# Optimization experiments

Measured on AMD Instinct MI355X. Metric: run time of the kernel, lower is better.

## Reference

```python
import jax, jax.numpy as jnp
import numpy as np

B, S, I, H = 64, 1024, 256, 256


def setup_inputs() -> dict:
    key = jax.random.key(0)
    ks = jax.random.split(key, 20)
    k = (1.0 / H) ** 0.5
    u = lambda kk, shape: jax.random.uniform(kk, shape, jnp.float32, -k, k)
    inp = {
        'inputs': jax.random.normal(ks[0], (B, S, I), jnp.float32),
        'h0': jax.random.normal(ks[1], (1, B, H), jnp.float32),
        'c0': jax.random.normal(ks[2], (1, B, H), jnp.float32),
        'w_ii': u(ks[3], (H, I)), 'w_if': u(ks[4], (H, I)),
        'w_ig': u(ks[5], (H, I)), 'w_io': u(ks[6], (H, I)),
        'b_ii': u(ks[7], (H,)), 'b_if': u(ks[8], (H,)),
        'b_ig': u(ks[9], (H,)), 'b_io': u(ks[10], (H,)),
        'w_hi': u(ks[11], (H, H)), 'w_hf': u(ks[12], (H, H)),
        'w_hg': u(ks[13], (H, H)), 'w_ho': u(ks[14], (H, H)),
        'b_hi': u(ks[15], (H,)), 'b_hf': u(ks[16], (H,)),
        'b_hg': u(ks[17], (H,)), 'b_ho': u(ks[18], (H,)),
    }
    return inp


def reference(inputs, h0, c0, w_ii, w_if, w_ig, w_io, b_ii, b_if, b_ig, b_io,
              w_hi, w_hf, w_hg, w_ho, b_hi, b_hf, b_hg, b_ho):
    # Precompute all input-to-gate projections over the whole sequence (one big GEMM each).
    # Shapes: [B, S, H] -> transposed to [S, B, H] for the time scan.
    xi = (jnp.einsum('bsi,hi->bsh', inputs, w_ii) + b_ii + b_hi).transpose(1, 0, 2)
    xf = (jnp.einsum('bsi,hi->bsh', inputs, w_if) + b_if + b_hf).transpose(1, 0, 2)
    xg = (jnp.einsum('bsi,hi->bsh', inputs, w_ig) + b_ig + b_hg).transpose(1, 0, 2)
    xo = (jnp.einsum('bsi,hi->bsh', inputs, w_io) + b_io + b_ho).transpose(1, 0, 2)

    def step(carry, xs):
        h, c = carry  # [B, H] each
        xi_t, xf_t, xg_t, xo_t = xs
        i_t = jax.nn.sigmoid(xi_t + h @ w_hi.T)
        f_t = jax.nn.sigmoid(xf_t + h @ w_hf.T)
        g_t = jnp.tanh(xg_t + h @ w_hg.T)
        o_t = jax.nn.sigmoid(xo_t + h @ w_ho.T)
        c = f_t * c + i_t * g_t
        h = o_t * jnp.tanh(c)
        return (h, c), h

    (hN, cN), hs = jax.lax.scan(step, (h0[0], c0[0]), (xi, xf, xg, xo))
    x = hs.transpose(1, 0, 2)  # [B, S, H]
    return x, (hN[None], cN[None])
```

## Files before the change

kernel.cpp:

```cpp
#include <hip/hip_runtime.h>
#include <hip/hip_fp16.h>
#include <stdint.h>


typedef __attribute__((ext_vector_type(4))) int v4i;
typedef __attribute__((ext_vector_type(4))) float f32x4;
typedef __attribute__((ext_vector_type(8))) short short8;
typedef __attribute__((ext_vector_type(2))) unsigned u32x2;

#define S_LEN 1024
#define HID 256
#define NB 64
#define PA 136
#define HP 288

__device__ __forceinline__ short f2bf(float f) {
  union { float f; unsigned u; } v; v.f = f;
  unsigned r = v.u + 0x7FFFu + ((v.u >> 16) & 1u);
  return (short)(r >> 16);
}

__device__ __forceinline__ float fsigm(float x) {
  return __builtin_amdgcn_rcpf(1.0f + __expf(-x));
}
__device__ __forceinline__ float ftanh(float x) {
  return 2.0f * __builtin_amdgcn_rcpf(1.0f + __expf(-2.0f * x)) - 1.0f;
}

__global__ __launch_bounds__(256) void conv_bf16(
    const float* __restrict__ inputs,
    const float* __restrict__ w_ii, const float* __restrict__ w_if,
    const float* __restrict__ w_ig, const float* __restrict__ w_io,
    unsigned short* __restrict__ Abf, unsigned short* __restrict__ Wbf) {
  const size_t NIN8 = (size_t)NB * S_LEN * HID / 8;
  const size_t NW8 = (size_t)4 * HID * HID / 8;
  size_t i = (size_t)blockIdx.x * 256 + threadIdx.x;
  const float* src;
  unsigned short* dst;
  if (i < NIN8) {
    src = inputs + i * 8;
    dst = Abf + i * 8;
  } else if (i < NIN8 + NW8) {
    size_t w8 = i - NIN8;
    int g = (int)(w8 >> 13);
    const float* Wg = (g == 0) ? w_ii : (g == 1) ? w_if : (g == 2) ? w_ig : w_io;
    src = Wg + (w8 & 8191) * 8;
    dst = Wbf + w8 * 8;
  } else {
    return;
  }
  float4 a = ((const float4*)src)[0];
  float4 b = ((const float4*)src)[1];
  union { short s[8]; short8 v; } pk;
  pk.s[0] = f2bf(a.x); pk.s[1] = f2bf(a.y); pk.s[2] = f2bf(a.z); pk.s[3] = f2bf(a.w);
  pk.s[4] = f2bf(b.x); pk.s[5] = f2bf(b.y); pk.s[6] = f2bf(b.z); pk.s[7] = f2bf(b.w);
  *(short8*)dst = pk.v;
}

__global__ __launch_bounds__(256) void lstm_xproj(
    const unsigned short* __restrict__ Abf, const unsigned short* __restrict__ Wbf,
    const float* __restrict__ b_ii, const float* __restrict__ b_if,
    const float* __restrict__ b_ig, const float* __restrict__ b_io,
    const float* __restrict__ b_hi, const float* __restrict__ b_hf,
    const float* __restrict__ b_hg, const float* __restrict__ b_ho,
    unsigned short* __restrict__ xacc, int t0, int TC) {
  __shared__ short Alds[64 * PA];
  __shared__ short Blds[64 * PA];

  const int tid = threadIdx.x;
  const int mt = blockIdx.x;
  const int g = blockIdx.y >> 2;
  const int jq = blockIdx.y & 3;

  const int b = (mt * 64) / TC;
  const int tl0 = (mt * 64) % TC;

  const float* B1 = (g == 0) ? b_ii : (g == 1) ? b_if : (g == 2) ? b_ig : b_io;
  const float* B2 = (g == 0) ? b_hi : (g == 1) ? b_hf : (g == 2) ? b_hg : b_ho;

  const int wv = tid >> 6;
  const int lane = tid & 63;
  const int jl = lane & 15;
  const int kg = lane >> 4;

  const int rr = tid >> 2;
  const int ks = (tid & 3) * 32;

  f32x4 acc[4] = {{0, 0, 0, 0}, {0, 0, 0, 0}, {0, 0, 0, 0}, {0, 0, 0, 0}};

  for (int kh = 0; kh < 2; ++kh) {
    __syncthreads();
    {
      const short8* src = (const short8*)(Abf +
          ((size_t)b * S_LEN + (t0 + tl0 + rr)) * HID + kh * 128 + ks);
      const short8* wsrc = (const short8*)(Wbf +
          (size_t)(g * HID + jq * 64 + rr) * HID + kh * 128 + ks);
#pragma unroll
      for (int i = 0; i < 4; ++i) {
        *(short8*)&Alds[rr * PA + ks + i * 8] = src[i];
        *(short8*)&Blds[rr * PA + ks + i * 8] = wsrc[i];
      }
    }
    __syncthreads();
#pragma unroll
    for (int kk = 0; kk < 4; ++kk) {
      short8 bfrag = *(const short8*)&Blds[(wv * 16 + jl) * PA + kk * 32 + kg * 8];
#pragma unroll
      for (int ms = 0; ms < 4; ++ms) {
        short8 afrag = *(const short8*)&Alds[(ms * 16 + jl) * PA + kk * 32 + kg * 8];
        acc[ms] = __builtin_amdgcn_mfma_f32_16x16x32_bf16(afrag, bfrag, acc[ms], 0, 0, 0);
      }
    }
  }

  const int j = jq * 64 + wv * 16 + jl;
  const float bias = B1[j] + B2[j];
  const int grp = b >> 4;
  const int brow = b & 15;
  const int r8 = brow & 3;
  const int Lp = jl + ((brow >> 2) << 4);
  const int jtg = jq * 4 + wv;

#pragma unroll
  for (int ms = 0; ms < 4; ++ms) {
#pragma unroll
    for (int ri = 0; ri < 4; ++ri) {
      int m = ms * 16 + kg * 4 + ri;
      int tl = tl0 + m;
      float v = acc[ms][ri] + bias;
      size_t a = ((size_t)(tl * 4 + grp) << 14) +
                 (size_t)((jtg * 64 + Lp) * 16 + r8 * 4 + g);
      xacc[a] = __half_as_ushort(__float2half(v));
    }
  }
}

__global__ __launch_bounds__(1024) void lstm_scan(
    const float* __restrict__ h0, const float* __restrict__ c0,
    const float* __restrict__ w_hi, const float* __restrict__ w_hf,
    const float* __restrict__ w_hg, const float* __restrict__ w_ho,
    float* __restrict__ out, const unsigned short* __restrict__ xacc,
    unsigned* __restrict__ ws_h8, float* __restrict__ ws_c,
    int t0, int TC) {
  __shared__ char h8[2][4 * HP];

  const int tid = threadIdx.x;
  const int jt = tid >> 6;
  const int lane = tid & 63;
  const int jl = lane & 15;
  const int kg = lane >> 4;
  const int ngrp = blockIdx.x;
  const int b = ngrp * 4 + kg;
  const int jc = jt * 16 + jl;

  const float* Wg4[4] = {w_hi, w_hf, w_hg, w_ho};
  v4i W8[16];
#pragma unroll
  for (int g = 0; g < 4; ++g) {
#pragma unroll
    for (int w = 0; w < 4; ++w) {
      const float4* p = (const float4*)(Wg4[g] +
          (size_t)jc * HID + w * 64 + kg * 16);
      int bb[16];
#pragma unroll
      for (int q = 0; q < 4; ++q) {
        float4 v = p[q];
        bb[q*4+0] = (int)fminf(fmaxf(rintf(v.x * 2032.f), -127.f), 127.f);
        bb[q*4+1] = (int)fminf(fmaxf(rintf(v.y * 2032.f), -127.f), 127.f);
        bb[q*4+2] = (int)fminf(fmaxf(rintf(v.z * 2032.f), -127.f), 127.f);
        bb[q*4+3] = (int)fminf(fmaxf(rintf(v.w * 2032.f), -127.f), 127.f);
      }
      v4i pk;
#pragma unroll
      for (int q = 0; q < 4; ++q)
        pk[q] = (bb[q*4+0] & 255) | ((bb[q*4+1] & 255) << 8) |
                ((bb[q*4+2] & 255) << 16) | ((bb[q*4+3] & 255) << 24);
      W8[g * 4 + w] = pk;
    }
  }

  float c;
  if (t0 == 0) c = c0[(size_t)b * HID + jc];
  else         c = ws_c[(size_t)b * HID + jc];

  if (t0 == 0) {
    if (tid < 256) {
      int row = tid >> 6;
      int cc = (tid & 63) * 4;
      float4 hv = *(const float4*)(h0 + (size_t)(ngrp * 4 + row) * HID + cc);
      int b0 = (int)fminf(fmaxf(rintf(hv.x * 31.75f), -127.f), 127.f);
      int b1 = (int)fminf(fmaxf(rintf(hv.y * 31.75f), -127.f), 127.f);
      int b2 = (int)fminf(fmaxf(rintf(hv.z * 31.75f), -127.f), 127.f);
      int b3 = (int)fminf(fmaxf(rintf(hv.w * 31.75f), -127.f), 127.f);
      *(int*)&h8[0][row * HP + cc] =
          (b0 & 255) | ((b1 & 255) << 8) | ((b2 & 255) << 16) | ((b3 & 255) << 24);
    }
  } else {
    if (tid < 256)
      *(unsigned*)&h8[t0 & 1][(tid >> 6) * HP + (tid & 63) * 4] =
          ws_h8[ngrp * 256 + tid];
  }
  __syncthreads();

  const float qn = 1.0f / (127.f * 2032.f);
  const float q0 = 1.0f / (31.75f * 2032.f);

  const unsigned short* xp = xacc + ((size_t)(ngrp >> 2) << 14) +
      (size_t)((jt * 64 + jl + ((ngrp & 3) << 4)) * 16 + kg * 4);
  float* outp = out + ((size_t)b * S_LEN + t0) * HID + jc;

  const int arow = (jl >> 2) * HP;

  for (int t = t0; t < t0 + TC; ++t) {
    const int cur = t & 1;
    const int nxt = cur ^ 1;

    u32x2 xv = *(const u32x2*)xp;
    xp += 65536;

    v4i acc[4];
#pragma unroll
    for (int g = 0; g < 4; ++g) acc[g] = (v4i){0, 0, 0, 0};
#pragma unroll
    for (int w = 0; w < 4; ++w) {
      v4i a = *(const v4i*)&h8[cur][arow + w * 64 + kg * 16];
#pragma unroll
      for (int g = 0; g < 4; ++g)
        acc[g] = __builtin_amdgcn_mfma_i32_16x16x64_i8(a, W8[g * 4 + w], acc[g], 0, 0, 0);
    }

    const float q = (t == 0) ? q0 : qn;
    const __half* xh = (const __half*)&xv;
    float pre_i = (float)acc[0][0] * q + __half2float(xh[0]);
    float pre_f = (float)acc[1][0] * q + __half2float(xh[1]);
    float pre_g = (float)acc[2][0] * q + __half2float(xh[2]);
    float pre_o = (float)acc[3][0] * q + __half2float(xh[3]);
    float iv = fsigm(pre_i);
    float fv = fsigm(pre_f);
    float gv = ftanh(pre_g);
    float ov = fsigm(pre_o);
    c = fv * c + iv * gv;
    float hh = ov * ftanh(c);

    *outp = hh;
    outp += HID;
    if (t == S_LEN - 1) {
      out[(size_t)NB * S_LEN * HID + (size_t)b * HID + jc] = hh;
      out[(size_t)NB * S_LEN * HID + (size_t)NB * HID + (size_t)b * HID + jc] = c;
    }
    int q8 = (int)fminf(fmaxf(rintf(hh * 127.f), -127.f), 127.f);
    h8[nxt][kg * HP + jc] = (char)q8;
    __syncthreads();
  }

  if (tid < 256)
    ws_h8[ngrp * 256 + tid] =
        *(const unsigned*)&h8[(t0 + TC) & 1][(tid >> 6) * HP + (tid & 63) * 4];
  ws_c[(size_t)b * HID + jc] = c;
}

extern "C" void kernel_launch(void* const* d_in, const int* in_sizes, int n_in,
                              void* d_out, int out_size, void* d_ws, size_t ws_size,
                              hipStream_t stream) {
  const float* inputs = (const float*)d_in[0];
  const float* h0 = (const float*)d_in[1];
  const float* c0 = (const float*)d_in[2];
  const float* w_ii = (const float*)d_in[3];
  const float* w_if = (const float*)d_in[4];
  const float* w_ig = (const float*)d_in[5];
  const float* w_io = (const float*)d_in[6];
  const float* b_ii = (const float*)d_in[7];
  const float* b_if = (const float*)d_in[8];
  const float* b_ig = (const float*)d_in[9];
  const float* b_io = (const float*)d_in[10];
  const float* w_hi = (const float*)d_in[11];
  const float* w_hf = (const float*)d_in[12];
  const float* w_hg = (const float*)d_in[13];
  const float* w_ho = (const float*)d_in[14];
  const float* b_hi = (const float*)d_in[15];
  const float* b_hf = (const float*)d_in[16];
  const float* b_hg = (const float*)d_in[17];
  const float* b_ho = (const float*)d_in[18];

  float* out = (float*)d_out;

  const size_t wb = (size_t)4 * HID * HID * 2;
  const size_t ab = (size_t)NB * S_LEN * HID * 2;
  const size_t base = wb + ab + 32768 + 65536;

  unsigned short* Wbf = (unsigned short*)d_ws;
  unsigned short* Abf = (unsigned short*)((char*)d_ws + wb);
  unsigned* ws_h8 = (unsigned*)((char*)d_ws + wb + ab);
  float* ws_c = (float*)((char*)d_ws + wb + ab + 32768);
  unsigned short* xacc = (unsigned short*)((char*)d_ws + base);

  int TC = 64;
  const int cands[5] = {1024, 512, 256, 128, 64};
  for (int i = 0; i < 5; ++i) {
    size_t need = base + (size_t)cands[i] * 131072;
    if (need <= ws_size) { TC = cands[i]; break; }
  }

  conv_bf16<<<8320, 256, 0, stream>>>(inputs, w_ii, w_if, w_ig, w_io, Abf, Wbf);

  for (int t0 = 0; t0 < S_LEN; t0 += TC) {
    lstm_xproj<<<dim3(TC, 16), 256, 0, stream>>>(
        Abf, Wbf,
        b_ii, b_if, b_ig, b_io, b_hi, b_hf, b_hg, b_ho,
        xacc, t0, TC);
    lstm_scan<<<16, 1024, 0, stream>>>(
        h0, c0, w_hi, w_hf, w_hg, w_ho,
        out, xacc, ws_h8, ws_c, t0, TC);
  }
}
```

Measured before the change: 1.335 ms.

## Retile input projection GEMM and stage output in LDS for coalesced stores

New measurement: 1.298 ms. 1.03x faster.

```diff
diff --git a/kernel.cpp b/kernel.cpp
--- a/kernel.cpp
+++ b/kernel.cpp
@@ -11,7 +11,7 @@
 #define S_LEN 1024
 #define HID 256
 #define NB 64
-#define PA 136
+#define PA 68
 #define HP 288
 
 __device__ __forceinline__ short f2bf(float f) {
@@ -64,74 +64,97 @@
     const float* __restrict__ b_hi, const float* __restrict__ b_hf,
     const float* __restrict__ b_hg, const float* __restrict__ b_ho,
     unsigned short* __restrict__ xacc, int t0, int TC) {
-  __shared__ short Alds[64 * PA];
-  __shared__ short Blds[64 * PA];
+  __shared__ short lds[2 * 128 * PA];
+  short* Alds = lds;
+  short* Blds = lds + 128 * PA;
+  unsigned short* Osh = (unsigned short*)lds;
 
   const int tid = threadIdx.x;
-  const int mt = blockIdx.x;
-  const int g = blockIdx.y >> 2;
-  const int jq = blockIdx.y & 3;
-
-  const int b = (mt * 64) / TC;
-  const int tl0 = (mt * 64) % TC;
-
-  const float* B1 = (g == 0) ? b_ii : (g == 1) ? b_if : (g == 2) ? b_ig : b_io;
-  const float* B2 = (g == 0) ? b_hi : (g == 1) ? b_hf : (g == 2) ? b_hg : b_ho;
+  const int bx = blockIdx.x;
+  const int jtgp = blockIdx.y;
+  const int grp = blockIdx.z;
 
   const int wv = tid >> 6;
   const int lane = tid & 63;
   const int jl = lane & 15;
   const int kg = lane >> 4;
 
-  const int rr = tid >> 2;
-  const int ks = (tid & 3) * 32;
-
-  f32x4 acc[4] = {{0, 0, 0, 0}, {0, 0, 0, 0}, {0, 0, 0, 0}, {0, 0, 0, 0}};
-
-  for (int kh = 0; kh < 2; ++kh) {
+  const int R = tid >> 1;
+  const int half = tid & 1;
+  const int bloc = R & 15;
+  const int tloc_s = R >> 4;
+
+  const unsigned short* asrc = Abf +
+      ((size_t)(grp * 16 + bloc) * S_LEN + (t0 + bx * 8 + tloc_s)) * HID + half * 32;
+  const int cS = R;
+  const unsigned short* bsrc = Wbf +
+      ((size_t)((cS & 3) * HID + jtgp * 32 + (cS >> 2))) * HID + half * 32;
+
+  f32x4 acc[2][8];
+#pragma unroll
+  for (int ms = 0; ms < 2; ++ms)
+#pragma unroll
+    for (int ct = 0; ct < 8; ++ct) acc[ms][ct] = (f32x4){0, 0, 0, 0};
+
+  for (int ks = 0; ks < HID; ks += 64) {
     __syncthreads();
-    {
-      const short8* src = (const short8*)(Abf +
-          ((size_t)b * S_LEN + (t0 + tl0 + rr)) * HID + kh * 128 + ks);
-      const short8* wsrc = (const short8*)(Wbf +
-          (size_t)(g * HID + jq * 64 + rr) * HID + kh * 128 + ks);
-#pragma unroll
-      for (int i = 0; i < 4; ++i) {
-        *(short8*)&Alds[rr * PA + ks + i * 8] = src[i];
-        *(short8*)&Blds[rr * PA + ks + i * 8] = wsrc[i];
+    short8 av[4], bv[4];
+#pragma unroll
+    for (int i = 0; i < 4; ++i) {
+      av[i] = *(const short8*)(asrc + ks + i * 8);
+      bv[i] = *(const short8*)(bsrc + ks + i * 8);
+    }
+#pragma unroll
+    for (int i = 0; i < 4; ++i) {
+      *(short8*)&Alds[R * PA + half * 32 + i * 8] = av[i];
+      *(short8*)&Blds[R * PA + half * 32 + i * 8] = bv[i];
+    }
+    __syncthreads();
+#pragma unroll
+    for (int kk = 0; kk < 2; ++kk) {
+      short8 af0 = *(const short8*)&Alds[((wv * 2 + 0) * 16 + jl) * PA + kk * 32 + kg * 8];
+      short8 af1 = *(const short8*)&Alds[((wv * 2 + 1) * 16 + jl) * PA + kk * 32 + kg * 8];
+#pragma unroll
+      for (int ct = 0; ct < 8; ++ct) {
+        short8 bf = *(const short8*)&Blds[(ct * 16 + jl) * PA + kk * 32 + kg * 8];
+        acc[0][ct] = __builtin_amdgcn_mfma_f32_16x16x32_bf16(af0, bf, acc[0][ct], 0, 0, 0);
+        acc[1][ct] = __builtin_amdgcn_mfma_f32_16x16x32_bf16(af1, bf, acc[1][ct], 0, 0, 0);
       }
     }
-    __syncthreads();
-#pragma unroll
-    for (int kk = 0; kk < 4; ++kk) {
-      short8 bfrag = *(const short8*)&Blds[(wv * 16 + jl) * PA + kk * 32 + kg * 8];
-#pragma unroll
-      for (int ms = 0; ms < 4; ++ms) {
-        short8 afrag = *(const short8*)&Alds[(ms * 16 + jl) * PA + kk * 32 + kg * 8];
-        acc[ms] = __builtin_amdgcn_mfma_f32_16x16x32_bf16(afrag, bfrag, acc[ms], 0, 0, 0);
+  }
+
+  const int g = jl & 3;
+  const float* B1g = (g == 0) ? b_ii : (g == 1) ? b_if : (g == 2) ? b_ig : b_io;
+  const float* B2g = (g == 0) ? b_hi : (g == 1) ? b_hf : (g == 2) ? b_hg : b_ho;
+  float bias[8];
+#pragma unroll
+  for (int ct = 0; ct < 8; ++ct) {
+    int j = jtgp * 32 + ct * 4 + (jl >> 2);
+    bias[ct] = B1g[j] + B2g[j];
+  }
+
+  __syncthreads();
+#pragma unroll
+  for (int ms = 0; ms < 2; ++ms) {
+    const int tloc = wv * 2 + ms;
+#pragma unroll
+    for (int ct = 0; ct < 8; ++ct) {
+      int jloc = ct * 4 + (jl >> 2);
+      int cb = ((jloc >> 4) << 10) + (jloc & 15) * 16 + kg * 256 + (jl & 3);
+#pragma unroll
+      for (int ri = 0; ri < 4; ++ri) {
+        float v = acc[ms][ct][ri] + bias[ct];
+        Osh[tloc * 2048 + cb + ri * 4] = __half_as_ushort(__float2half(v));
       }
     }
   }
-
-  const int j = jq * 64 + wv * 16 + jl;
-  const float bias = B1[j] + B2[j];
-  const int grp = b >> 4;
-  const int brow = b & 15;
-  const int r8 = brow & 3;
-  const int Lp = jl + ((brow >> 2) << 4);
-  const int jtg = jq * 4 + wv;
-
-#pragma unroll
-  for (int ms = 0; ms < 4; ++ms) {
-#pragma unroll
-    for (int ri = 0; ri < 4; ++ri) {
-      int m = ms * 16 + kg * 4 + ri;
-      int tl = tl0 + m;
-      float v = acc[ms][ri] + bias;
-      size_t a = ((size_t)(tl * 4 + grp) << 14) +
-                 (size_t)((jtg * 64 + Lp) * 16 + r8 * 4 + g);
-      xacc[a] = __half_as_ushort(__float2half(v));
-    }
+  __syncthreads();
+
+#pragma unroll
+  for (int t2 = 0; t2 < 8; ++t2) {
+    int tl = bx * 8 + t2;
+    *(short8*)(xacc + (((size_t)(tl * 4 + grp)) << 14) + jtgp * 2048 + tid * 8) =
+        *(const short8*)&Osh[t2 * 2048 + tid * 8];
   }
 }
 
@@ -304,7 +327,7 @@
   conv_bf16<<<8320, 256, 0, stream>>>(inputs, w_ii, w_if, w_ig, w_io, Abf, Wbf);
 
   for (int t0 = 0; t0 < S_LEN; t0 += TC) {
-    lstm_xproj<<<dim3(TC, 16), 256, 0, stream>>>(
+    lstm_xproj<<<dim3(TC / 8, 8, 4), 256, 0, stream>>>(
         Abf, Wbf,
         b_ii, b_if, b_ig, b_io, b_hi, b_hf, b_hg, b_ho,
         xacc, t0, TC);
```
